# Kernel optimization log

Hardware: AMD Instinct MI355X
Metric: run time of the kernel (lower is better)

Reference implementation:

```python
import jax, jax.numpy as jnp
import numpy as np

INPUT_SIZE = 128
HIDDEN = 1024
CATEGORIES = 50


def setup_inputs() -> dict:
    key = jax.random.key(0)
    ks = jax.random.split(key, 16)
    stdv = 1.0 / np.sqrt(HIDDEN)

    def u(k, shape):
        return jax.random.uniform(k, shape, jnp.float32, -stdv, stdv)

    inp = {
        "x": jax.random.normal(ks[0], (128, 1000, INPUT_SIZE), jnp.float32),
        "W_ii": u(ks[1], (INPUT_SIZE, HIDDEN)),
        "W_hi": u(ks[2], (HIDDEN, HIDDEN)),
        "b_ii": u(ks[3], (HIDDEN,)),
        "W_if": u(ks[4], (INPUT_SIZE, HIDDEN)),
        "W_hf": u(ks[5], (HIDDEN, HIDDEN)),
        "b_if": jnp.ones((HIDDEN,), jnp.float32),  # forget bias init to 1
        "W_ig": u(ks[6], (INPUT_SIZE, HIDDEN)),
        "W_hg": u(ks[7], (HIDDEN, HIDDEN)),
        "b_ig": u(ks[8], (HIDDEN,)),
        "W_io": u(ks[9], (INPUT_SIZE, HIDDEN)),
        "W_ho": u(ks[10], (HIDDEN, HIDDEN)),
        "b_io": u(ks[11], (HIDDEN,)),
        "W_out": u(ks[12], (CATEGORIES, HIDDEN)),  # nn.Linear weight layout
        "b_out": u(ks[13], (CATEGORIES,)),
    }
    return inp


def _lstm_last_h(x, W_ii, W_hi, b_ii, W_if, W_hf, b_if, W_ig, W_hg, b_ig, W_io, W_ho, b_io):
    B, S, _ = x.shape
    H = W_hi.shape[0]
    # Fuse the 4 input-projection GEMMs into one big GEMM over all timesteps.
    Wx = jnp.concatenate([W_ii, W_if, W_ig, W_io], axis=1)   # [I, 4H]
    Wh = jnp.concatenate([W_hi, W_hf, W_hg, W_ho], axis=1)   # [H, 4H]
    b = jnp.concatenate([b_ii, b_if, b_ig, b_io], axis=0)    # [4H]
    xg = jnp.einsum('bsi,ij->sbj', x, Wx) + b                # [S, B, 4H]

    def step(carry, g_x):
        h, c = carry
        g = g_x + h @ Wh                                      # [B, 4H]
        i = jax.nn.sigmoid(g[:, 0*H:1*H])
        f = jax.nn.sigmoid(g[:, 1*H:2*H])
        gg = jnp.tanh(g[:, 2*H:3*H])
        o = jax.nn.sigmoid(g[:, 3*H:4*H])
        c = f * c + i * gg
        h = o * jnp.tanh(c)
        return (h, c), None

    h0 = jnp.zeros((B, H), x.dtype)
    c0 = jnp.zeros((B, H), x.dtype)
    (h_t, _), _ = jax.lax.scan(step, (h0, c0), xg)
    return h_t


def reference(x, W_ii, W_hi, b_ii, W_if, W_hf, b_if, W_ig, W_hg, b_ig,
              W_io, W_ho, b_io, W_out, b_out):
    h_t = _lstm_last_h(x, W_ii, W_hi, b_ii, W_if, W_hf, b_if,
                       W_ig, W_hg, b_ig, W_io, W_ho, b_io)
    return h_t @ W_out.T + b_out  # [B, categories]
```

## Files before the change

### kernel.cpp

```cpp
#include <hip/hip_runtime.h>
#include <hip/hip_bf16.h>

#define BB 128
#define SS 1000
#define II 128
#define HH 1024
#define G4 4096
#define KK (II + HH)
#define NC 50
#define NB 256
#define SPIN_LIM (1 << 20)

typedef __attribute__((ext_vector_type(8))) short short8v;
typedef __attribute__((ext_vector_type(4))) float f32x4;

static __device__ __forceinline__ short f2bf(float f) {
    union { float f; unsigned u; } v; v.f = f;
    unsigned u = v.u;
    u += 0x7FFFu + ((u >> 16) & 1u);
    return (short)(u >> 16);
}

__global__ void prep_weights(const float* __restrict__ Wx0, const float* __restrict__ Wx1,
                             const float* __restrict__ Wx2, const float* __restrict__ Wx3,
                             const float* __restrict__ Wh0, const float* __restrict__ Wh1,
                             const float* __restrict__ Wh2, const float* __restrict__ Wh3,
                             short* __restrict__ Bt) {
    __shared__ float lds[32][33];
    const int kt = blockIdx.x, jt = blockIdx.y, g = blockIdx.z;
    const int tx = threadIdx.x, ty = threadIdx.y;
    const float* Wx = (g == 0) ? Wx0 : (g == 1) ? Wx1 : (g == 2) ? Wx2 : Wx3;
    const float* Wh = (g == 0) ? Wh0 : (g == 1) ? Wh1 : (g == 2) ? Wh2 : Wh3;
    const int k0 = kt * 32, j0 = jt * 32;
#pragma unroll
    for (int r = 0; r < 4; r++) {
        int kk = k0 + ty + r * 8;
        float v = (kk < II) ? Wx[kk * HH + j0 + tx] : Wh[(kk - II) * HH + j0 + tx];
        lds[ty + r * 8][tx] = v;
    }
    __syncthreads();
#pragma unroll
    for (int r = 0; r < 4; r++) {
        int jj = ty + r * 8;
        Bt[(size_t)(g * HH + j0 + jj) * KK + k0 + tx] = f2bf(lds[tx][jj]);
    }
}

__global__ void prep_misc(const float* __restrict__ bi, const float* __restrict__ bf_,
                          const float* __restrict__ bg, const float* __restrict__ bo,
                          float* __restrict__ b4, short* __restrict__ hbuf,
                          unsigned* __restrict__ flags) {
    int i = blockIdx.x * 256 + threadIdx.x;
    if (i < G4) {
        float v = (i < HH) ? bi[i] : (i < 2 * HH) ? bf_[i - HH]
                : (i < 3 * HH) ? bg[i - 2 * HH] : bo[i - 3 * HH];
        b4[i] = v;
    }
    if (i < BB * HH) hbuf[i] = 0;
    if (i < 1024) flags[i] = 0;
}

__global__ __launch_bounds__(256, 1) void lstm_persist(
    const float* __restrict__ x, const short* __restrict__ Bt,
    const float* __restrict__ b4, short* __restrict__ hbuf,
    float* __restrict__ hf, unsigned* __restrict__ flags) {
    const int bid = blockIdx.x;
    const int mg = bid & 7, jg = bid >> 3;
    const int m0 = mg * 16, j0 = jg * 32;
    const int tid = threadIdx.x;
    const int g = tid >> 6, l = tid & 63;
    const int lq = l >> 4, lr = l & 15;
    unsigned* gflags = flags + mg * 64;

    __shared__ __align__(16) short hstage[16 * 1024];
    __shared__ float g4s[4][16][33];
    __shared__ float c_lds[16][33];
    __shared__ int dead;

    if (tid == 0) dead = 0;
    for (int i = tid; i < 16 * 33; i += 256) ((float*)c_lds)[i] = 0.f;

    short8v Bw[36][2];
    {
        const short* Bg = Bt + (size_t)(g * HH + j0) * KK;
#pragma unroll
        for (int kk = 0; kk < 36; kk++) {
#pragma unroll
            for (int nt = 0; nt < 2; nt++) {
                Bw[kk][nt] = *(const short8v*)(Bg + (size_t)(nt * 16 + lr) * KK + kk * 32 + lq * 8);
            }
        }
    }

    const int arow = m0 + lr;
    const float* xrow = x + (size_t)arow * SS * II;

    const int m_e = tid >> 4;
    const int j2 = (tid & 15) * 2;
    const float bi0 = b4[j0 + j2],          bi1 = b4[j0 + j2 + 1];
    const float bf0 = b4[HH + j0 + j2],     bf1 = b4[HH + j0 + j2 + 1];
    const float bg0 = b4[2 * HH + j0 + j2], bg1 = b4[2 * HH + j0 + j2 + 1];
    const float bo0 = b4[3 * HH + j0 + j2], bo1 = b4[3 * HH + j0 + j2 + 1];

    __syncthreads();

    f32x4 acc0 = {0.f, 0.f, 0.f, 0.f}, acc1 = acc0;

#pragma unroll
    for (int kk = 0; kk < 4; kk++) {
        const float4* xp = (const float4*)(xrow + kk * 32 + lq * 8);
        float4 x0 = xp[0], x1 = xp[1];
        short8v a;
        a[0] = f2bf(x0.x); a[1] = f2bf(x0.y); a[2] = f2bf(x0.z); a[3] = f2bf(x0.w);
        a[4] = f2bf(x1.x); a[5] = f2bf(x1.y); a[6] = f2bf(x1.z); a[7] = f2bf(x1.w);
        acc0 = __builtin_amdgcn_mfma_f32_16x16x32_bf16(a, Bw[kk][0], acc0, 0, 0, 0);
        acc1 = __builtin_amdgcn_mfma_f32_16x16x32_bf16(a, Bw[kk][1], acc1, 0, 0, 0);
    }

    for (int t = 0; t < SS; t++) {
        const short* hcur = hbuf + (size_t)(t & 1) * (BB * HH);
        short* hnxt = hbuf + (size_t)((t + 1) & 1) * (BB * HH);

        if (!dead && tid < 32) {
            const unsigned e = (unsigned)t;
            int it = 0;
            while (__hip_atomic_load(&gflags[tid], __ATOMIC_RELAXED,
                                     __HIP_MEMORY_SCOPE_AGENT) < e) {
                if (++it > SPIN_LIM) { dead = 1; break; }
            }
        }
        __syncthreads();

        {
            const unsigned long long* hsrc =
                (const unsigned long long*)(hcur + (size_t)m0 * HH);
            unsigned long long v[16];
#pragma unroll
            for (int it = 0; it < 16; it++)
                v[it] = __hip_atomic_load(hsrc + it * 256 + tid,
                                          __ATOMIC_RELAXED, __HIP_MEMORY_SCOPE_AGENT);
#pragma unroll
            for (int it = 0; it < 16; it++) {
                int off = (tid * 8) ^ ((it & 7) << 4);
                *(unsigned long long*)((char*)hstage + it * 2048 + off) = v[it];
            }
        }
        __syncthreads();

#pragma unroll
        for (int kk2 = 0; kk2 < 32; kk2++) {
            short8v a = *(const short8v*)((const char*)hstage + lr * 2048 +
                                          ((kk2 * 64 + lq * 16) ^ ((lr & 7) << 4)));
            acc0 = __builtin_amdgcn_mfma_f32_16x16x32_bf16(a, Bw[kk2 + 4][0], acc0, 0, 0, 0);
            acc1 = __builtin_amdgcn_mfma_f32_16x16x32_bf16(a, Bw[kk2 + 4][1], acc1, 0, 0, 0);
        }

#pragma unroll
        for (int r = 0; r < 4; r++) {
            g4s[g][lq * 4 + r][lr] = acc0[r];
            g4s[g][lq * 4 + r][16 + lr] = acc1[r];
        }
        __syncthreads();

        {
            float gi0 = g4s[0][m_e][j2] + bi0, gi1 = g4s[0][m_e][j2 + 1] + bi1;
            float gf0 = g4s[1][m_e][j2] + bf0, gf1 = g4s[1][m_e][j2 + 1] + bf1;
            float gg0 = g4s[2][m_e][j2] + bg0, gg1 = g4s[2][m_e][j2 + 1] + bg1;
            float go0 = g4s[3][m_e][j2] + bo0, go1 = g4s[3][m_e][j2 + 1] + bo1;
            float si0 = 1.f / (1.f + __expf(-gi0)), si1 = 1.f / (1.f + __expf(-gi1));
            float sf0 = 1.f / (1.f + __expf(-gf0)), sf1 = 1.f / (1.f + __expf(-gf1));
            float tg0 = 1.f - 2.f / (__expf(2.f * gg0) + 1.f);
            float tg1 = 1.f - 2.f / (__expf(2.f * gg1) + 1.f);
            float so0 = 1.f / (1.f + __expf(-go0)), so1 = 1.f / (1.f + __expf(-go1));
            float cn0 = sf0 * c_lds[m_e][j2] + si0 * tg0;
            float cn1 = sf1 * c_lds[m_e][j2 + 1] + si1 * tg1;
            c_lds[m_e][j2] = cn0;
            c_lds[m_e][j2 + 1] = cn1;
            float h0 = so0 * (1.f - 2.f / (__expf(2.f * cn0) + 1.f));
            float h1 = so1 * (1.f - 2.f / (__expf(2.f * cn1) + 1.f));
            unsigned pv = (unsigned)(unsigned short)f2bf(h0)
                        | ((unsigned)(unsigned short)f2bf(h1) << 16);
            unsigned* hp = (unsigned*)(hnxt + (size_t)(m0 + m_e) * HH + j0 + j2);
            __hip_atomic_store(hp, pv, __ATOMIC_RELAXED, __HIP_MEMORY_SCOPE_AGENT);
            if (t == SS - 1) {
                float2 hv = make_float2(h0, h1);
                *(float2*)(hf + (size_t)(m0 + m_e) * HH + j0 + j2) = hv;
            }
        }

        if (t == SS - 1) break;

        __syncthreads();
        if (!dead && tid == 0)
            __hip_atomic_store(&gflags[jg], (unsigned)(t + 1),
                               __ATOMIC_RELAXED, __HIP_MEMORY_SCOPE_AGENT);

        acc0 = f32x4{0.f, 0.f, 0.f, 0.f}; acc1 = acc0;
        {
            const float* xt = xrow + (size_t)(t + 1) * II;
#pragma unroll
            for (int kk = 0; kk < 4; kk++) {
                const float4* xp = (const float4*)(xt + kk * 32 + lq * 8);
                float4 x0 = xp[0], x1 = xp[1];
                short8v a;
                a[0] = f2bf(x0.x); a[1] = f2bf(x0.y); a[2] = f2bf(x0.z); a[3] = f2bf(x0.w);
                a[4] = f2bf(x1.x); a[5] = f2bf(x1.y); a[6] = f2bf(x1.z); a[7] = f2bf(x1.w);
                acc0 = __builtin_amdgcn_mfma_f32_16x16x32_bf16(a, Bw[kk][0], acc0, 0, 0, 0);
                acc1 = __builtin_amdgcn_mfma_f32_16x16x32_bf16(a, Bw[kk][1], acc1, 0, 0, 0);
            }
        }
    }

    (void)dead;
}

__global__ void final_linear(const float* __restrict__ hf, const float* __restrict__ Wout,
                             const float* __restrict__ bout, float* __restrict__ out) {
    __shared__ float hs[HH];
    const int b = blockIdx.x;
    for (int i = threadIdx.x; i < HH; i += 256) hs[i] = hf[(size_t)b * HH + i];
    __syncthreads();
    const int w = threadIdx.x >> 6, l = threadIdx.x & 63;
    for (int o = w; o < NC; o += 4) {
        float s = 0.f;
        const float* wr = Wout + (size_t)o * HH;
        for (int jj = l; jj < HH; jj += 64) s += hs[jj] * wr[jj];
#pragma unroll
        for (int d = 32; d > 0; d >>= 1) s += __shfl_down(s, d);
        if (l == 0) out[b * NC + o] = s + bout[o];
    }
}

extern "C" void kernel_launch(void* const* d_in, const int* in_sizes, int n_in,
                              void* d_out, int out_size, void* d_ws, size_t ws_size,
                              hipStream_t stream) {
    const float* x    = (const float*)d_in[0];
    const float* W_ii = (const float*)d_in[1];
    const float* W_hi = (const float*)d_in[2];
    const float* b_ii = (const float*)d_in[3];
    const float* W_if = (const float*)d_in[4];
    const float* W_hf = (const float*)d_in[5];
    const float* b_if = (const float*)d_in[6];
    const float* W_ig = (const float*)d_in[7];
    const float* W_hg = (const float*)d_in[8];
    const float* b_ig = (const float*)d_in[9];
    const float* W_io = (const float*)d_in[10];
    const float* W_ho = (const float*)d_in[11];
    const float* b_io = (const float*)d_in[12];
    const float* W_out = (const float*)d_in[13];
    const float* b_out = (const float*)d_in[14];

    char* ws = (char*)d_ws;
    short* Bt   = (short*)ws;
    float* b4   = (float*)(ws + 9437184);
    short* hbuf = (short*)(ws + 9437184 + 16384);
    float* hf   = (float*)(ws + 9437184 + 16384 + 524288);
    unsigned* flags = (unsigned*)(ws + 9437184 + 16384 + 524288 + 524288);

    prep_weights<<<dim3(36, 32, 4), dim3(32, 8), 0, stream>>>(
        W_ii, W_if, W_ig, W_io, W_hi, W_hf, W_hg, W_ho, Bt);
    prep_misc<<<512, 256, 0, stream>>>(b_ii, b_if, b_ig, b_io, b4, hbuf, flags);

    lstm_persist<<<NB, 256, 0, stream>>>(x, Bt, b4, hbuf, hf, flags);

    final_linear<<<BB, 256, 0, stream>>>(hf, W_out, b_out, (float*)d_out);
}
```

Baseline: 4.701 ms.

## Replace per-group step flags with epoch-tagged hidden-state words

Each bf16 pair of the hidden state is now stored as a 64-bit word that carries the timestep in its upper half. Consumers poll the data words directly instead of waiting on per-block flags, which removes the flag spin, the extra barrier and the flag store from the critical path of every step. The final hidden state is read back from the tagged words as bf16, so the last output loses the fp32 copy. The cost is that global hidden-state traffic doubles and each element gets its own retry loop.

Result: slower. 5.188 ms (+10.4%).

```diff
diff --git a/kernel.cpp b/kernel.cpp
--- a/kernel.cpp
+++ b/kernel.cpp
@@ -9,17 +9,17 @@
 #define KK (II + HH)
 #define NC 50
 #define NB 256
-#define SPIN_LIM (1 << 20)
 
 typedef __attribute__((ext_vector_type(8))) short short8v;
 typedef __attribute__((ext_vector_type(4))) float f32x4;
 
-static __device__ __forceinline__ short f2bf(float f) {
+static __device__ __forceinline__ unsigned f2bfu(float f) {
     union { float f; unsigned u; } v; v.f = f;
     unsigned u = v.u;
     u += 0x7FFFu + ((u >> 16) & 1u);
-    return (short)(u >> 16);
-}
+    return u >> 16;
+}
+static __device__ __forceinline__ short f2bf(float f) { return (short)f2bfu(f); }
 
 __global__ void prep_weights(const float* __restrict__ Wx0, const float* __restrict__ Wx1,
                              const float* __restrict__ Wx2, const float* __restrict__ Wx3,
@@ -48,29 +48,25 @@
 
 __global__ void prep_misc(const float* __restrict__ bi, const float* __restrict__ bf_,
                           const float* __restrict__ bg, const float* __restrict__ bo,
-                          float* __restrict__ b4, short* __restrict__ hbuf,
-                          unsigned* __restrict__ flags) {
+                          float* __restrict__ b4, unsigned long long* __restrict__ hw) {
     int i = blockIdx.x * 256 + threadIdx.x;
     if (i < G4) {
         float v = (i < HH) ? bi[i] : (i < 2 * HH) ? bf_[i - HH]
                 : (i < 3 * HH) ? bg[i - 2 * HH] : bo[i - 3 * HH];
         b4[i] = v;
     }
-    if (i < BB * HH) hbuf[i] = 0;
-    if (i < 1024) flags[i] = 0;
+    if (i < 2 * BB * 512) hw[i] = 0ull;
 }
 
 __global__ __launch_bounds__(256, 1) void lstm_persist(
     const float* __restrict__ x, const short* __restrict__ Bt,
-    const float* __restrict__ b4, short* __restrict__ hbuf,
-    float* __restrict__ hf, unsigned* __restrict__ flags) {
+    const float* __restrict__ b4, unsigned long long* __restrict__ hw) {
     const int bid = blockIdx.x;
     const int mg = bid & 7, jg = bid >> 3;
     const int m0 = mg * 16, j0 = jg * 32;
     const int tid = threadIdx.x;
     const int g = tid >> 6, l = tid & 63;
     const int lq = l >> 4, lr = l & 15;
-    unsigned* gflags = flags + mg * 64;
 
     __shared__ __align__(16) short hstage[16 * 1024];
     __shared__ float g4s[4][16][33];
@@ -101,6 +97,7 @@
     const float bf0 = b4[HH + j0 + j2],     bf1 = b4[HH + j0 + j2 + 1];
     const float bg0 = b4[2 * HH + j0 + j2], bg1 = b4[2 * HH + j0 + j2 + 1];
     const float bo0 = b4[3 * HH + j0 + j2], bo1 = b4[3 * HH + j0 + j2 + 1];
+    unsigned long long* const myword0 = hw + (size_t)(m0 + m_e) * 512 + ((j0 + j2) >> 1);
 
     __syncthreads();
 
@@ -118,31 +115,44 @@
     }
 
     for (int t = 0; t < SS; t++) {
-        const short* hcur = hbuf + (size_t)(t & 1) * (BB * HH);
-        short* hnxt = hbuf + (size_t)((t + 1) & 1) * (BB * HH);
-
-        if (!dead && tid < 32) {
-            const unsigned e = (unsigned)t;
-            int it = 0;
-            while (__hip_atomic_load(&gflags[tid], __ATOMIC_RELAXED,
-                                     __HIP_MEMORY_SCOPE_AGENT) < e) {
-                if (++it > SPIN_LIM) { dead = 1; break; }
-            }
-        }
-        __syncthreads();
-
-        {
-            const unsigned long long* hsrc =
-                (const unsigned long long*)(hcur + (size_t)m0 * HH);
+        const unsigned et = (unsigned)t;
+        const unsigned long long* wbase = hw + (size_t)(t & 1) * (BB * 512) + (size_t)m0 * 512;
+
+#pragma unroll
+        for (int p = 0; p < 2; p++) {
             unsigned long long v[16];
 #pragma unroll
-            for (int it = 0; it < 16; it++)
-                v[it] = __hip_atomic_load(hsrc + it * 256 + tid,
-                                          __ATOMIC_RELAXED, __HIP_MEMORY_SCOPE_AGENT);
-#pragma unroll
-            for (int it = 0; it < 16; it++) {
-                int off = (tid * 8) ^ ((it & 7) << 4);
-                *(unsigned long long*)((char*)hstage + it * 2048 + off) = v[it];
+            for (int q = 0; q < 16; q++)
+                v[q] = __hip_atomic_load(wbase + (p * 16 + q) * 256 + tid,
+                                         __ATOMIC_RELAXED, __HIP_MEMORY_SCOPE_AGENT);
+            unsigned pend = 0;
+#pragma unroll
+            for (int q = 0; q < 16; q++) {
+                const int it = p * 16 + q;
+                const int row = it >> 1, c2 = ((it & 1) << 8) + tid;
+                if ((unsigned)(v[q] >> 32) == et) {
+                    *(unsigned*)((char*)hstage + row * 2048 + ((c2 * 4) ^ ((row & 7) << 4)))
+                        = (unsigned)v[q];
+                } else pend |= 1u << q;
+            }
+            int guard = 0;
+            while (pend && !dead) {
+#pragma unroll
+                for (int q = 0; q < 16; q++) {
+                    if (pend & (1u << q)) {
+                        unsigned long long nv = __hip_atomic_load(
+                            wbase + (p * 16 + q) * 256 + tid,
+                            __ATOMIC_RELAXED, __HIP_MEMORY_SCOPE_AGENT);
+                        if ((unsigned)(nv >> 32) == et) {
+                            const int it = p * 16 + q;
+                            const int row = it >> 1, c2 = ((it & 1) << 8) + tid;
+                            *(unsigned*)((char*)hstage + row * 2048 +
+                                         ((c2 * 4) ^ ((row & 7) << 4))) = (unsigned)nv;
+                            pend &= ~(1u << q);
+                        }
+                    }
+                }
+                if (++guard > (1 << 16)) dead = 1;
             }
         }
         __syncthreads();
@@ -178,22 +188,14 @@
             c_lds[m_e][j2 + 1] = cn1;
             float h0 = so0 * (1.f - 2.f / (__expf(2.f * cn0) + 1.f));
             float h1 = so1 * (1.f - 2.f / (__expf(2.f * cn1) + 1.f));
-            unsigned pv = (unsigned)(unsigned short)f2bf(h0)
-                        | ((unsigned)(unsigned short)f2bf(h1) << 16);
-            unsigned* hp = (unsigned*)(hnxt + (size_t)(m0 + m_e) * HH + j0 + j2);
-            __hip_atomic_store(hp, pv, __ATOMIC_RELAXED, __HIP_MEMORY_SCOPE_AGENT);
-            if (t == SS - 1) {
-                float2 hv = make_float2(h0, h1);
-                *(float2*)(hf + (size_t)(m0 + m_e) * HH + j0 + j2) = hv;
-            }
+            unsigned pay = f2bfu(h0) | (f2bfu(h1) << 16);
+            unsigned long long word =
+                ((unsigned long long)(unsigned)(t + 1) << 32) | (unsigned long long)pay;
+            __hip_atomic_store(myword0 + (size_t)(((t + 1) & 1)) * (BB * 512), word,
+                               __ATOMIC_RELAXED, __HIP_MEMORY_SCOPE_AGENT);
         }
 
         if (t == SS - 1) break;
-
-        __syncthreads();
-        if (!dead && tid == 0)
-            __hip_atomic_store(&gflags[jg], (unsigned)(t + 1),
-                               __ATOMIC_RELAXED, __HIP_MEMORY_SCOPE_AGENT);
 
         acc0 = f32x4{0.f, 0.f, 0.f, 0.f}; acc1 = acc0;
         {
@@ -209,16 +211,25 @@
                 acc1 = __builtin_amdgcn_mfma_f32_16x16x32_bf16(a, Bw[kk][1], acc1, 0, 0, 0);
             }
         }
+        __syncthreads();
     }
 
     (void)dead;
 }
 
-__global__ void final_linear(const float* __restrict__ hf, const float* __restrict__ Wout,
+__global__ void final_linear(const unsigned long long* __restrict__ hw,
+                             const float* __restrict__ Wout,
                              const float* __restrict__ bout, float* __restrict__ out) {
     __shared__ float hs[HH];
     const int b = blockIdx.x;
-    for (int i = threadIdx.x; i < HH; i += 256) hs[i] = hf[(size_t)b * HH + i];
+    for (int i = threadIdx.x; i < 512; i += 256) {
+        unsigned pay = (unsigned)hw[(size_t)b * 512 + i];
+        union { unsigned u; float f; } lo, hi;
+        lo.u = (pay & 0xFFFFu) << 16;
+        hi.u = (pay & 0xFFFF0000u);
+        hs[2 * i] = lo.f;
+        hs[2 * i + 1] = hi.f;
+    }
     __syncthreads();
     const int w = threadIdx.x >> 6, l = threadIdx.x & 63;
     for (int o = w; o < NC; o += 4) {
@@ -251,17 +262,16 @@
     const float* b_out = (const float*)d_in[14];
 
     char* ws = (char*)d_ws;
-    short* Bt   = (short*)ws;
-    float* b4   = (float*)(ws + 9437184);
-    short* hbuf = (short*)(ws + 9437184 + 16384);
-    float* hf   = (float*)(ws + 9437184 + 16384 + 524288);
-    unsigned* flags = (unsigned*)(ws + 9437184 + 16384 + 524288 + 524288);
+    short* Bt = (short*)ws;
+    float* b4 = (float*)(ws + 9437184);
+    unsigned long long* hw =
+        (unsigned long long*)(ws + 9437184 + 16384);
 
     prep_weights<<<dim3(36, 32, 4), dim3(32, 8), 0, stream>>>(
         W_ii, W_if, W_ig, W_io, W_hi, W_hf, W_hg, W_ho, Bt);
-    prep_misc<<<512, 256, 0, stream>>>(b_ii, b_if, b_ig, b_io, b4, hbuf, flags);
-
-    lstm_persist<<<NB, 256, 0, stream>>>(x, Bt, b4, hbuf, hf, flags);
-
-    final_linear<<<BB, 256, 0, stream>>>(hf, W_out, b_out, (float*)d_out);
-}
+    prep_misc<<<512, 256, 0, stream>>>(b_ii, b_if, b_ig, b_io, b4, hw);
+
+    lstm_persist<<<NB, 256, 0, stream>>>(x, Bt, b4, hw);
+
+    final_linear<<<BB, 256, 0, stream>>>(hw, W_out, b_out, (float*)d_out);
+}
```

## Use XCD-local cache-scoped loads/stores when a batch group shares one XCD

Applied to the files above, without the earlier changes.

Each block reads its hardware XCC ID and publishes it. The blocks of each batch group then check whether all of them landed on the same XCD. If they did, the spin-wait flag loads and hidden-state loads use sc0-scoped global loads instead of agent-scope atomics, and the stores become plain volatile stores. The goal is to cut per-step handoff latency by keeping the step-to-step sync traffic in the XCD-local L2 instead of going through device-coherent paths. It depends on block-to-XCD placement, adds an extra startup handshake, and relies on memory-ordering assumptions that could be fragile.

Result: slower. 5.065 ms (+7.7%).

```diff
diff --git a/kernel.cpp b/kernel.cpp
--- a/kernel.cpp
+++ b/kernel.cpp
@@ -14,12 +14,13 @@
 typedef __attribute__((ext_vector_type(8))) short short8v;
 typedef __attribute__((ext_vector_type(4))) float f32x4;
 
-static __device__ __forceinline__ short f2bf(float f) {
+static __device__ __forceinline__ unsigned f2bfu(float f) {
     union { float f; unsigned u; } v; v.f = f;
     unsigned u = v.u;
     u += 0x7FFFu + ((u >> 16) & 1u);
-    return (short)(u >> 16);
-}
+    return u >> 16;
+}
+static __device__ __forceinline__ short f2bf(float f) { return (short)f2bfu(f); }
 
 __global__ void prep_weights(const float* __restrict__ Wx0, const float* __restrict__ Wx1,
                              const float* __restrict__ Wx2, const float* __restrict__ Wx3,
@@ -71,14 +72,21 @@
     const int g = tid >> 6, l = tid & 63;
     const int lq = l >> 4, lr = l & 15;
     unsigned* gflags = flags + mg * 64;
+    unsigned* xcdids = flags + 512;
 
     __shared__ __align__(16) short hstage[16 * 1024];
     __shared__ float g4s[4][16][33];
     __shared__ float c_lds[16][33];
     __shared__ int dead;
+    __shared__ int fastflag;
 
     if (tid == 0) dead = 0;
     for (int i = tid; i < 16 * 33; i += 256) ((float*)c_lds)[i] = 0.f;
+
+    unsigned xcc = 0;
+    asm volatile("s_getreg_b32 %0, hwreg(HW_REG_XCC_ID)" : "=s"(xcc));
+    if (tid == 0)
+        __hip_atomic_store(&xcdids[bid], xcc + 1, __ATOMIC_RELAXED, __HIP_MEMORY_SCOPE_AGENT);
 
     short8v Bw[36][2];
     {
@@ -90,6 +98,17 @@
                 Bw[kk][nt] = *(const short8v*)(Bg + (size_t)(nt * 16 + lr) * KK + kk * 32 + lq * 8);
             }
         }
+    }
+
+    if (tid < 64) {
+        unsigned pv = 0; int gu = 0;
+        do {
+            pv = __hip_atomic_load(&xcdids[mg + (tid & 31) * 8],
+                                   __ATOMIC_RELAXED, __HIP_MEMORY_SCOPE_AGENT);
+        } while (pv == 0 && ++gu <= SPIN_LIM);
+        unsigned ref = __builtin_amdgcn_readfirstlane(pv);
+        unsigned long long mask = __ballot(pv != 0 && pv == ref);
+        if (tid == 0) fastflag = (mask == ~0ull) ? 1 : 0;
     }
 
     const int arow = m0 + lr;
@@ -103,6 +122,7 @@
     const float bo0 = b4[3 * HH + j0 + j2], bo1 = b4[3 * HH + j0 + j2 + 1];
 
     __syncthreads();
+    const bool fastp = (fastflag != 0);
 
     f32x4 acc0 = {0.f, 0.f, 0.f, 0.f}, acc1 = acc0;
 
@@ -123,11 +143,20 @@
 
         if (!dead && tid < 32) {
             const unsigned e = (unsigned)t;
-            int it = 0;
-            while (__hip_atomic_load(&gflags[tid], __ATOMIC_RELAXED,
-                                     __HIP_MEMORY_SCOPE_AGENT) < e) {
-                if (++it > SPIN_LIM) { dead = 1; break; }
-            }
+            unsigned fv; int it = 0;
+            if (fastp) {
+                const unsigned* fp_ = &gflags[tid];
+                do {
+                    asm volatile("global_load_dword %0, %1, off sc0\n\ts_waitcnt vmcnt(0)"
+                                 : "=v"(fv) : "v"(fp_) : "memory");
+                } while (fv < e && ++it <= SPIN_LIM);
+            } else {
+                do {
+                    fv = __hip_atomic_load(&gflags[tid], __ATOMIC_RELAXED,
+                                           __HIP_MEMORY_SCOPE_AGENT);
+                } while (fv < e && ++it <= SPIN_LIM);
+            }
+            if (it > SPIN_LIM) dead = 1;
         }
         __syncthreads();
 
@@ -135,14 +164,25 @@
             const unsigned long long* hsrc =
                 (const unsigned long long*)(hcur + (size_t)m0 * HH);
             unsigned long long v[16];
-#pragma unroll
-            for (int it = 0; it < 16; it++)
-                v[it] = __hip_atomic_load(hsrc + it * 256 + tid,
-                                          __ATOMIC_RELAXED, __HIP_MEMORY_SCOPE_AGENT);
-#pragma unroll
-            for (int it = 0; it < 16; it++) {
-                int off = (tid * 8) ^ ((it & 7) << 4);
-                *(unsigned long long*)((char*)hstage + it * 2048 + off) = v[it];
+            if (fastp) {
+#pragma unroll
+                for (int q = 0; q < 16; q++) {
+                    const unsigned long long* p = hsrc + q * 256 + tid;
+                    asm volatile("global_load_dwordx2 %0, %1, off sc0"
+                                 : "=v"(v[q]) : "v"(p));
+                }
+                asm volatile("s_waitcnt vmcnt(0)" ::: "memory");
+                __builtin_amdgcn_sched_barrier(0);
+            } else {
+#pragma unroll
+                for (int q = 0; q < 16; q++)
+                    v[q] = __hip_atomic_load(hsrc + q * 256 + tid,
+                                             __ATOMIC_RELAXED, __HIP_MEMORY_SCOPE_AGENT);
+            }
+#pragma unroll
+            for (int q = 0; q < 16; q++) {
+                int off = (tid * 8) ^ ((q & 7) << 4);
+                *(unsigned long long*)((char*)hstage + q * 2048 + off) = v[q];
             }
         }
         __syncthreads();
@@ -178,10 +218,10 @@
             c_lds[m_e][j2 + 1] = cn1;
             float h0 = so0 * (1.f - 2.f / (__expf(2.f * cn0) + 1.f));
             float h1 = so1 * (1.f - 2.f / (__expf(2.f * cn1) + 1.f));
-            unsigned pv = (unsigned)(unsigned short)f2bf(h0)
-                        | ((unsigned)(unsigned short)f2bf(h1) << 16);
+            unsigned pv = f2bfu(h0) | (f2bfu(h1) << 16);
             unsigned* hp = (unsigned*)(hnxt + (size_t)(m0 + m_e) * HH + j0 + j2);
-            __hip_atomic_store(hp, pv, __ATOMIC_RELAXED, __HIP_MEMORY_SCOPE_AGENT);
+            if (fastp) *(volatile unsigned*)hp = pv;
+            else __hip_atomic_store(hp, pv, __ATOMIC_RELAXED, __HIP_MEMORY_SCOPE_AGENT);
             if (t == SS - 1) {
                 float2 hv = make_float2(h0, h1);
                 *(float2*)(hf + (size_t)(m0 + m_e) * HH + j0 + j2) = hv;
@@ -190,10 +230,13 @@
 
         if (t == SS - 1) break;
 
+        asm volatile("s_waitcnt vmcnt(0)" ::: "memory");
         __syncthreads();
-        if (!dead && tid == 0)
-            __hip_atomic_store(&gflags[jg], (unsigned)(t + 1),
-                               __ATOMIC_RELAXED, __HIP_MEMORY_SCOPE_AGENT);
+        if (!dead && tid == 0) {
+            if (fastp) *(volatile unsigned*)&gflags[jg] = (unsigned)(t + 1);
+            else __hip_atomic_store(&gflags[jg], (unsigned)(t + 1),
+                                    __ATOMIC_RELAXED, __HIP_MEMORY_SCOPE_AGENT);
+        }
 
         acc0 = f32x4{0.f, 0.f, 0.f, 0.f}; acc1 = acc0;
         {
```
